# Performance work log

Hardware: AMD Instinct MI355X
Metric: run time of the kernel (lower is better)

## Reference

```python
import jax, jax.numpy as jnp
import numpy as np

N_NODES = 100000
N_EDGES = 1600000
DIM = 128
N_SEEDS = 15000


def _gcn_stack(edges, x, Ws):
    """Multi-layer GCN with sym-normalized edge-list aggregation, residual, ReLU.
    edges: [2, E] int; x: [N, d] float; Ws: list of [d, d] weights."""
    n = x.shape[0]
    loop = jnp.arange(n, dtype=edges.dtype)
    src = jnp.concatenate([edges[0], loop])  # add self-loops
    dst = jnp.concatenate([edges[1], loop])
    deg = jax.ops.segment_sum(jnp.ones(src.shape, x.dtype), dst, num_segments=n)
    dinv = jax.lax.rsqrt(deg)  # deg >= 1 thanks to self-loops
    norm = dinv[src] * dinv[dst]  # [E+N]
    for W in Ws:
        h = x @ W                                   # [N, d] dense transform
        msg = norm[:, None] * h[src]                # gather + scale, [E+N, d]
        agg = jax.ops.segment_sum(msg, dst, num_segments=n)  # scatter-add
        x = jax.nn.relu(agg + h)                    # residual + activation
    return x


def setup_inputs() -> dict:
    key = jax.random.key(0)
    ks = jax.random.split(key, 8)
    scale = 1.0 / np.sqrt(DIM)
    return {
        "sr_ent_seeds": jax.random.randint(ks[0], (N_SEEDS,), 0, N_NODES),
        "tg_ent_seeds": jax.random.randint(ks[1], (N_SEEDS,), 0, N_NODES),
        "edges_sr": jax.random.randint(ks[2], (2, N_EDGES), 0, N_NODES),
        "edges_tg": jax.random.randint(ks[3], (2, N_EDGES), 0, N_NODES),
        "embedding_sr": jax.random.normal(ks[4], (N_NODES, DIM), jnp.float32),
        "embedding_tg": jax.random.normal(ks[5], (N_NODES, DIM), jnp.float32),
        "W0": jax.random.normal(ks[6], (DIM, DIM), jnp.float32) * scale,
        "W1": jax.random.normal(ks[7], (DIM, DIM), jnp.float32) * scale,
    }


def reference(sr_ent_seeds, tg_ent_seeds, edges_sr, edges_tg,
              embedding_sr, embedding_tg, W0, W1):
    Ws = [W0, W1]
    sr_ent_hid = _gcn_stack(edges_sr, embedding_sr, Ws)
    tg_ent_hid = _gcn_stack(edges_tg, embedding_tg, Ws)
    sr_seed_hid = sr_ent_hid[sr_ent_seeds]
    tg_seed_hid = tg_ent_hid[tg_ent_seeds]
    return (sr_seed_hid, tg_seed_hid, sr_ent_hid, tg_ent_hid)
```

## Files before the change

### kernel.cpp

```cpp
#include <hip/hip_runtime.h>

#define NN 100000
#define NE 1600000
#define NT (2 * NN)
#define ET (2 * NE)
#define DIM 128
#define NS 15000
#define SB2 ((NT + 255) / 256)
#define PAD 136
#define NRANGE 16
#define RSZ (NT / NRANGE)
#define CH 16
#define BCAP 210000
#define NE4 (NE / 4)

typedef __attribute__((ext_vector_type(8))) short frag_ab;
typedef __attribute__((ext_vector_type(4))) float frag_cd;
typedef __attribute__((ext_vector_type(4))) int i4;
typedef __attribute__((ext_vector_type(2))) float f32x2;

__device__ __forceinline__ unsigned short f2bf(float f) {
    unsigned int u = __float_as_uint(f);
    u += 0x7fff + ((u >> 16) & 1);
    return (unsigned short)(u >> 16);
}
__device__ __forceinline__ float bflo(unsigned int u) { return __uint_as_float(u << 16); }
__device__ __forceinline__ float bfhi(unsigned int u) { return __uint_as_float(u & 0xffff0000u); }

__global__ __launch_bounds__(256) void bucket_k(const int* __restrict__ e_sr,
                                                const int* __restrict__ e_tg,
                                                int* __restrict__ gcur,
                                                int* __restrict__ bkt) {
    __shared__ int bcnt[4][NRANGE];
    __shared__ int bbase[4][NRANGE];
    const int tid = threadIdx.x;
    if (tid < 4 * NRANGE) ((int*)bcnt)[tid] = 0;
    __syncthreads();
    const int g = blockIdx.x * 256 + tid;
    i4 s4, d4;
    if (g < NE4) {
        s4 = *((const i4*)e_sr + g);
        d4 = *((const i4*)e_sr + NE4 + g);
    } else {
        s4 = *((const i4*)e_tg + g - NE4);
        d4 = *((const i4*)e_tg + g);
        s4 += NN;
        d4 += NN;
    }
    const int wv = tid >> 6;
    int rr[4], lr[4];
#pragma unroll
    for (int j = 0; j < 4; ++j) {
        rr[j] = d4[j] / RSZ;
        lr[j] = atomicAdd(&bcnt[wv][rr[j]], 1);
    }
    __syncthreads();
    if (tid < NRANGE) {
        const int t0 = bcnt[0][tid], t1 = bcnt[1][tid];
        const int t2 = bcnt[2][tid], t3 = bcnt[3][tid];
        const int b = atomicAdd(&gcur[tid], t0 + t1 + t2 + t3);
        bbase[0][tid] = b;
        bbase[1][tid] = b + t0;
        bbase[2][tid] = b + t0 + t1;
        bbase[3][tid] = b + t0 + t1 + t2;
    }
    __syncthreads();
#pragma unroll
    for (int j = 0; j < 4; ++j) {
        const int dtl = d4[j] - rr[j] * RSZ;
        bkt[bbase[wv][rr[j]] + lr[j]] = (dtl << 18) | s4[j];
    }
}

__global__ __launch_bounds__(1024) void hist_k(const int* __restrict__ gcur,
                                               const int* __restrict__ bkt,
                                               int* __restrict__ P) {
    __shared__ int lc[RSZ];
    const int r = blockIdx.x & (NRANGE - 1);
    const int c = blockIdx.x >> 4;
    const int lo = r * RSZ;
    for (int i = threadIdx.x; i < RSZ; i += 1024) lc[i] = 0;
    __syncthreads();
    const int n_r = gcur[r] - r * BCAP;
    const int S = (n_r + CH - 1) / CH;
    const int s0 = c * S;
    int s1 = s0 + S; if (s1 > n_r) s1 = n_r;
    for (int v = s0 + threadIdx.x; v < s1; v += 1024) {
        const unsigned int w = (unsigned int)bkt[r * BCAP + v];
        atomicAdd(&lc[w >> 18], 1);
    }
    __syncthreads();
    for (int i = threadIdx.x; i < RSZ; i += 1024) P[c * NT + lo + i] = lc[i];
}

__global__ __launch_bounds__(256) void reduceA_k(const int* __restrict__ P,
                                                 int* __restrict__ cnt,
                                                 float* __restrict__ dinv,
                                                 int* __restrict__ bsum) {
    __shared__ int sh[256];
    const int t = threadIdx.x;
    const int i = blockIdx.x * 256 + t;
    int s = 0;
    if (i < NT) {
#pragma unroll
        for (int c = 0; c < CH; ++c) s += P[c * NT + i];
        cnt[i] = s;
        dinv[i] = rsqrtf((float)(s + 1));
    }
    sh[t] = s;
    __syncthreads();
    for (int off = 128; off > 0; off >>= 1) {
        if (t < off) sh[t] += sh[t + off];
        __syncthreads();
    }
    if (t == 0) bsum[blockIdx.x] = sh[0];
}

__global__ __launch_bounds__(256) void scanCbase_k(const int* __restrict__ cnt,
                                                   const int* __restrict__ bsum,
                                                   int* __restrict__ row_ptr,
                                                   int* __restrict__ P) {
    __shared__ int s[256];
    const int t = threadIdx.x;
    const int i = blockIdx.x * 256 + t;
    int acc = 0;
    for (int b = t; b < blockIdx.x; b += 256) acc += bsum[b];
    s[t] = acc;
    __syncthreads();
    for (int off = 128; off > 0; off >>= 1) {
        if (t < off) s[t] += s[t + off];
        __syncthreads();
    }
    const int boff = s[0];
    __syncthreads();
    const int v = (i < NT) ? cnt[i] : 0;
    s[t] = v;
    __syncthreads();
    for (int off = 1; off < 256; off <<= 1) {
        int add = (t >= off) ? s[t - off] : 0;
        __syncthreads();
        s[t] += add;
        __syncthreads();
    }
    if (blockIdx.x == 0 && t == 0) row_ptr[NT] = ET;
    if (i < NT) {
        const int rp = boff + s[t] - v;
        row_ptr[i] = rp;
        int run = rp;
#pragma unroll
        for (int c = 0; c < CH; ++c) {
            const int pv = P[c * NT + i];
            P[c * NT + i] = run;
            run += pv;
        }
    }
}

__global__ __launch_bounds__(1024) void fillp_k(const int* __restrict__ gcur,
                                                const int* __restrict__ bkt,
                                                const int* __restrict__ P,
                                                int* __restrict__ csr_src) {
    __shared__ int cur[RSZ];
    const int r = blockIdx.x & (NRANGE - 1);
    const int c = blockIdx.x >> 4;
    const int lo = r * RSZ;
    for (int i = threadIdx.x; i < RSZ; i += 1024) cur[i] = P[c * NT + lo + i];
    __syncthreads();
    const int n_r = gcur[r] - r * BCAP;
    const int S = (n_r + CH - 1) / CH;
    const int s0 = c * S;
    int s1 = s0 + S; if (s1 > n_r) s1 = n_r;
    for (int v = s0 + threadIdx.x; v < s1; v += 1024) {
        const unsigned int w = (unsigned int)bkt[r * BCAP + v];
        const int pos = atomicAdd(&cur[w >> 18], 1);
        csr_src[pos] = (int)(w & 0x3FFFFu);
    }
}

__global__ __launch_bounds__(256) void convW2_k(const float* __restrict__ W0,
                                                const float* __restrict__ W1,
                                                unsigned short* __restrict__ wt0,
                                                unsigned short* __restrict__ wt1,
                                                int* __restrict__ gcur) {
    int i = blockIdx.x * 256 + threadIdx.x;
    if (blockIdx.x == 0 && threadIdx.x < NRANGE) gcur[threadIdx.x] = threadIdx.x * BCAP;
    if (i >= 2 * DIM * DIM) return;
    const float* W = (i < DIM * DIM) ? W0 : W1;
    unsigned short* wt = (i < DIM * DIM) ? wt0 : wt1;
    const int ii = i & (DIM * DIM - 1);
    const int n = ii & 127, k = ii >> 7;
    wt[n * DIM + k] = f2bf(W[k * DIM + n]);
}

__global__ __launch_bounds__(256) void gemmE_k(const float* __restrict__ emb_sr,
                                               const float* __restrict__ emb_tg,
                                               const unsigned short* __restrict__ Wt,
                                               const float* __restrict__ dinv,
                                               unsigned short* __restrict__ Gb) {
    __shared__ unsigned short xs[64 * PAD];
    __shared__ unsigned short ws[128 * PAD];
    const int tid = threadIdx.x;
    const int row0 = blockIdx.x * 64;

    for (int i = tid; i < 128 * 16; i += 256) {
        const int r = i >> 4, o = i & 15;
        *(uint4*)&ws[r * PAD + o * 8] = *(const uint4*)&Wt[r * DIM + o * 8];
    }
    for (int i = tid; i < 64 * 32; i += 256) {
        const int r = i >> 5, o = i & 31;
        const int gr = row0 + r;
        const float4 v = (gr < NN) ? ((const float4*)emb_sr)[gr * 32 + o]
                                   : ((const float4*)emb_tg)[(gr - NN) * 32 + o];
        ushort4 b;
        b.x = f2bf(v.x); b.y = f2bf(v.y); b.z = f2bf(v.z); b.w = f2bf(v.w);
        *(ushort4*)&xs[r * PAD + o * 4] = b;
    }
    __syncthreads();

    const int wave = tid >> 6;
    const int lane = tid & 63;
    const int m = lane & 15;
    const int quad = lane >> 4;
    const int rbase = wave * 16;

    frag_cd acc[8];
#pragma unroll
    for (int ct = 0; ct < 8; ct++) acc[ct] = (frag_cd){0.f, 0.f, 0.f, 0.f};

#pragma unroll
    for (int ks = 0; ks < 4; ks++) {
        const frag_ab a = *(const frag_ab*)&xs[(rbase + m) * PAD + ks * 32 + quad * 8];
#pragma unroll
        for (int ct = 0; ct < 8; ct++) {
            const frag_ab b = *(const frag_ab*)&ws[(ct * 16 + m) * PAD + ks * 32 + quad * 8];
            acc[ct] = __builtin_amdgcn_mfma_f32_16x16x32_bf16(a, b, acc[ct], 0, 0, 0);
        }
    }

#pragma unroll
    for (int r = 0; r < 4; r++) {
        const int grow = row0 + rbase + quad * 4 + r;
        const float dv = dinv[grow];
#pragma unroll
        for (int ct = 0; ct < 8; ct++)
            Gb[grow * DIM + ct * 16 + m] = f2bf(dv * acc[ct][r]);
    }
}

__global__ __launch_bounds__(256) void gemm_mfma_k(const unsigned short* __restrict__ Xb,
                                                   const unsigned short* __restrict__ Wt,
                                                   const float* __restrict__ dinv,
                                                   unsigned short* __restrict__ Gb) {
    __shared__ unsigned short xs[64 * PAD];
    __shared__ unsigned short ws[128 * PAD];
    const int tid = threadIdx.x;
    const int row0 = blockIdx.x * 64;

    for (int i = tid; i < 128 * 16; i += 256) {
        const int r = i >> 4, o = i & 15;
        *(uint4*)&ws[r * PAD + o * 8] = *(const uint4*)&Wt[r * DIM + o * 8];
    }
    for (int i = tid; i < 64 * 16; i += 256) {
        const int r = i >> 4, o = i & 15;
        *(uint4*)&xs[r * PAD + o * 8] = *(const uint4*)&Xb[(row0 + r) * DIM + o * 8];
    }
    __syncthreads();

    const int wave = tid >> 6;
    const int lane = tid & 63;
    const int m = lane & 15;
    const int quad = lane >> 4;
    const int rbase = wave * 16;

    frag_cd acc[8];
#pragma unroll
    for (int ct = 0; ct < 8; ct++) acc[ct] = (frag_cd){0.f, 0.f, 0.f, 0.f};

#pragma unroll
    for (int ks = 0; ks < 4; ks++) {
        const frag_ab a = *(const frag_ab*)&xs[(rbase + m) * PAD + ks * 32 + quad * 8];
#pragma unroll
        for (int ct = 0; ct < 8; ct++) {
            const frag_ab b = *(const frag_ab*)&ws[(ct * 16 + m) * PAD + ks * 32 + quad * 8];
            acc[ct] = __builtin_amdgcn_mfma_f32_16x16x32_bf16(a, b, acc[ct], 0, 0, 0);
        }
    }

#pragma unroll
    for (int r = 0; r < 4; r++) {
        const int grow = row0 + rbase + quad * 4 + r;
        const float dv = dinv[grow];
#pragma unroll
        for (int ct = 0; ct < 8; ct++)
            Gb[grow * DIM + ct * 16 + m] = f2bf(dv * acc[ct][r]);
    }
}

template <bool OUT_BF16>
__global__ __launch_bounds__(256) void pull_k(const int* __restrict__ row_ptr,
                                              const int* __restrict__ csr_src,
                                              const float* __restrict__ dinv,
                                              const unsigned short* __restrict__ Gb,
                                              float* __restrict__ outf,
                                              unsigned short* __restrict__ outb) {
    const int node = (blockIdx.x * 256 + threadIdx.x) >> 6;
    if (node >= NT) return;
    const int lane = threadIdx.x & 63;
    const unsigned int* __restrict__ G2 = (const unsigned int*)Gb;

    const int beg = row_ptr[node];
    const int end = row_ptr[node + 1];
    const float d = dinv[node];
    const float sq = 1.0f / d;

    const unsigned int gu = G2[node * 64 + lane];
    float sx = bflo(gu);
    float sy = bfhi(gu);
    const float hx = sx * sq;
    const float hy = sy * sq;

    for (int base = beg; base < end; base += 64) {
        int rem = end - base; if (rem > 64) rem = 64;
        const int sl = (lane < rem)
            ? __builtin_nontemporal_load(&csr_src[base + lane]) : 0;
        int j = 0;
        for (; j + 16 <= rem; j += 16) {
            int ss[16];
            unsigned int mm[16];
#pragma unroll
            for (int q = 0; q < 16; ++q) ss[q] = __shfl(sl, j + q);
#pragma unroll
            for (int q = 0; q < 16; ++q) mm[q] = G2[ss[q] * 64 + lane];
#pragma unroll
            for (int q = 0; q < 16; ++q) { sx += bflo(mm[q]); sy += bfhi(mm[q]); }
        }
        for (; j + 8 <= rem; j += 8) {
            int ss[8];
            unsigned int mm[8];
#pragma unroll
            for (int q = 0; q < 8; ++q) ss[q] = __shfl(sl, j + q);
#pragma unroll
            for (int q = 0; q < 8; ++q) mm[q] = G2[ss[q] * 64 + lane];
#pragma unroll
            for (int q = 0; q < 8; ++q) { sx += bflo(mm[q]); sy += bfhi(mm[q]); }
        }
        for (; j + 4 <= rem; j += 4) {
            int ss[4];
            unsigned int mm[4];
#pragma unroll
            for (int q = 0; q < 4; ++q) ss[q] = __shfl(sl, j + q);
#pragma unroll
            for (int q = 0; q < 4; ++q) mm[q] = G2[ss[q] * 64 + lane];
#pragma unroll
            for (int q = 0; q < 4; ++q) { sx += bflo(mm[q]); sy += bfhi(mm[q]); }
        }
        for (; j < rem; ++j) {
            const int s = __shfl(sl, j);
            const unsigned int mu = G2[s * 64 + lane];
            sx += bflo(mu);
            sy += bfhi(mu);
        }
    }
    const float ax = fmaxf(d * sx + hx, 0.f);
    const float ay = fmaxf(d * sy + hy, 0.f);
    if (OUT_BF16) {
        const unsigned int o =
            (unsigned int)f2bf(ax) | ((unsigned int)f2bf(ay) << 16);
        __builtin_nontemporal_store(o, &((unsigned int*)outb)[node * 64 + lane]);
    } else {
        f32x2 o; o.x = ax; o.y = ay;
        __builtin_nontemporal_store(o, &((f32x2*)outf)[node * 64 + lane]);
    }
}

__global__ __launch_bounds__(256) void gather2_k(const int* __restrict__ sr_seeds,
                                                 const int* __restrict__ tg_seeds,
                                                 const float* __restrict__ ent,
                                                 float* __restrict__ sr_out,
                                                 float* __restrict__ tg_out) {
    const int gid = blockIdx.x * 256 + threadIdx.x;
    const int s = gid >> 5;
    if (s >= 2 * NS) return;
    const int q = gid & 31;
    const bool tg = s >= NS;
    const int si = tg ? s - NS : s;
    const int node = tg ? tg_seeds[si] + NN : sr_seeds[si];
    float* o = tg ? tg_out : sr_out;
    ((float4*)o)[si * 32 + q] = ((const float4*)ent)[node * 32 + q];
}

extern "C" void kernel_launch(void* const* d_in, const int* in_sizes, int n_in,
                              void* d_out, int out_size, void* d_ws, size_t ws_size,
                              hipStream_t stream) {
    const int* sr_seeds = (const int*)d_in[0];
    const int* tg_seeds = (const int*)d_in[1];
    const int* edges_sr = (const int*)d_in[2];
    const int* edges_tg = (const int*)d_in[3];
    const float* emb_sr = (const float*)d_in[4];
    const float* emb_tg = (const float*)d_in[5];
    const float* W0 = (const float*)d_in[6];
    const float* W1 = (const float*)d_in[7];
    float* out = (float*)d_out;

    int* cnt = (int*)d_ws;
    float* dinv = (float*)(cnt + 200704);
    int* row_ptr = (int*)(dinv + 200704);
    int* bsum = row_ptr + 200704;
    int* csr_src = bsum + 1024;
    unsigned short* wt0 = (unsigned short*)(csr_src + ET);
    unsigned short* wt1 = wt0 + DIM * DIM;
    unsigned short* hb = wt1 + DIM * DIM;
    int* P = (int*)hb;
    int* bkt = P + CH * NT;
    int* gcur = bsum + 800;

    float* sr_seed_out = out;
    float* tg_seed_out = out + (long long)NS * DIM;
    float* ent = out + (long long)2 * NS * DIM;
    unsigned short* xb = (unsigned short*)ent;

    const int gGemm = (NT + 63) / 64;
    const int gPull = NT / 4;
    const int gBkt = ET / 1024;
    const int gHF = NRANGE * CH;

    convW2_k<<<(2 * DIM * DIM + 255) / 256, 256, 0, stream>>>(W0, W1, wt0, wt1, gcur);

    bucket_k<<<gBkt, 256, 0, stream>>>(edges_sr, edges_tg, gcur, bkt);
    hist_k<<<gHF, 1024, 0, stream>>>(gcur, bkt, P);
    reduceA_k<<<SB2, 256, 0, stream>>>(P, cnt, dinv, bsum);
    scanCbase_k<<<SB2, 256, 0, stream>>>(cnt, bsum, row_ptr, P);
    fillp_k<<<gHF, 1024, 0, stream>>>(gcur, bkt, P, csr_src);

    gemmE_k<<<gGemm, 256, 0, stream>>>(emb_sr, emb_tg, wt0, dinv, hb);
    pull_k<true><<<gPull, 256, 0, stream>>>(row_ptr, csr_src, dinv, hb, nullptr, xb);
    gemm_mfma_k<<<gGemm, 256, 0, stream>>>(xb, wt1, dinv, hb);
    pull_k<false><<<gPull, 256, 0, stream>>>(row_ptr, csr_src, dinv, hb, ent, nullptr);

    const int gSeed = (2 * NS * 32 + 255) / 256;
    gather2_k<<<gSeed, 256, 0, stream>>>(sr_seeds, tg_seeds, ent, sr_seed_out, tg_seed_out);
}
```

Baseline: 576.8 us.

## Merge CSR build kernels into one cooperative kernel with grid syncs

Replaces the six preprocessing launches (weight convert, bucket, histogram, reduce, scan, fill) with a single cooperative kernel of 256 blocks by 1024 threads that separates the phases with grid-wide syncs. Buckets now use a per-range base offset with a zeroed counter set by a memset. The goal is to remove kernel launch gaps and tail effects between the small phases. In exchange, the bucketing phase runs in grid-stride loops with extra block barriers, and the cooperative launch limits the grid to co-resident blocks.

```diff
diff --git a/kernel.cpp b/kernel.cpp
--- a/kernel.cpp
+++ b/kernel.cpp
@@ -1,4 +1,7 @@
 #include <hip/hip_runtime.h>
+#include <hip/hip_cooperative_groups.h>
+
+namespace cg = cooperative_groups;
 
 #define NN 100000
 #define NE 1600000
@@ -6,13 +9,14 @@
 #define ET (2 * NE)
 #define DIM 128
 #define NS 15000
-#define SB2 ((NT + 255) / 256)
 #define PAD 136
 #define NRANGE 16
 #define RSZ (NT / NRANGE)
 #define CH 16
 #define BCAP 210000
 #define NE4 (NE / 4)
+#define CGRID 256
+#define CTHR 1024
 
 typedef __attribute__((ext_vector_type(8))) short frag_ab;
 typedef __attribute__((ext_vector_type(4))) float frag_cd;
@@ -27,169 +31,169 @@
 __device__ __forceinline__ float bflo(unsigned int u) { return __uint_as_float(u << 16); }
 __device__ __forceinline__ float bfhi(unsigned int u) { return __uint_as_float(u & 0xffff0000u); }
 
-__global__ __launch_bounds__(256) void bucket_k(const int* __restrict__ e_sr,
-                                                const int* __restrict__ e_tg,
-                                                int* __restrict__ gcur,
-                                                int* __restrict__ bkt) {
-    __shared__ int bcnt[4][NRANGE];
-    __shared__ int bbase[4][NRANGE];
+__global__ __launch_bounds__(CTHR) void csr_coop_k(
+    const float* __restrict__ W0, const float* __restrict__ W1,
+    unsigned short* __restrict__ wt0, unsigned short* __restrict__ wt1,
+    const int* __restrict__ e_sr, const int* __restrict__ e_tg,
+    int* __restrict__ gcur, int* __restrict__ bkt, int* __restrict__ P,
+    int* __restrict__ cnt, float* __restrict__ dinv, int* __restrict__ bsum,
+    int* __restrict__ row_ptr, int* __restrict__ csr_src)
+{
+    cg::grid_group grid = cg::this_grid();
+    __shared__ int lds_i[RSZ];
+    __shared__ int bcnt[16][NRANGE];
+    __shared__ int bbase[16][NRANGE];
     const int tid = threadIdx.x;
-    if (tid < 4 * NRANGE) ((int*)bcnt)[tid] = 0;
-    __syncthreads();
-    const int g = blockIdx.x * 256 + tid;
-    i4 s4, d4;
-    if (g < NE4) {
-        s4 = *((const i4*)e_sr + g);
-        d4 = *((const i4*)e_sr + NE4 + g);
-    } else {
-        s4 = *((const i4*)e_tg + g - NE4);
-        d4 = *((const i4*)e_tg + g);
-        s4 += NN;
-        d4 += NN;
-    }
-    const int wv = tid >> 6;
-    int rr[4], lr[4];
-#pragma unroll
-    for (int j = 0; j < 4; ++j) {
-        rr[j] = d4[j] / RSZ;
-        lr[j] = atomicAdd(&bcnt[wv][rr[j]], 1);
-    }
-    __syncthreads();
-    if (tid < NRANGE) {
-        const int t0 = bcnt[0][tid], t1 = bcnt[1][tid];
-        const int t2 = bcnt[2][tid], t3 = bcnt[3][tid];
-        const int b = atomicAdd(&gcur[tid], t0 + t1 + t2 + t3);
-        bbase[0][tid] = b;
-        bbase[1][tid] = b + t0;
-        bbase[2][tid] = b + t0 + t1;
-        bbase[3][tid] = b + t0 + t1 + t2;
-    }
-    __syncthreads();
-#pragma unroll
-    for (int j = 0; j < 4; ++j) {
-        const int dtl = d4[j] - rr[j] * RSZ;
-        bkt[bbase[wv][rr[j]] + lr[j]] = (dtl << 18) | s4[j];
-    }
-}
-
-__global__ __launch_bounds__(1024) void hist_k(const int* __restrict__ gcur,
-                                               const int* __restrict__ bkt,
-                                               int* __restrict__ P) {
-    __shared__ int lc[RSZ];
-    const int r = blockIdx.x & (NRANGE - 1);
-    const int c = blockIdx.x >> 4;
-    const int lo = r * RSZ;
-    for (int i = threadIdx.x; i < RSZ; i += 1024) lc[i] = 0;
-    __syncthreads();
-    const int n_r = gcur[r] - r * BCAP;
-    const int S = (n_r + CH - 1) / CH;
-    const int s0 = c * S;
-    int s1 = s0 + S; if (s1 > n_r) s1 = n_r;
-    for (int v = s0 + threadIdx.x; v < s1; v += 1024) {
-        const unsigned int w = (unsigned int)bkt[r * BCAP + v];
-        atomicAdd(&lc[w >> 18], 1);
-    }
-    __syncthreads();
-    for (int i = threadIdx.x; i < RSZ; i += 1024) P[c * NT + lo + i] = lc[i];
-}
-
-__global__ __launch_bounds__(256) void reduceA_k(const int* __restrict__ P,
-                                                 int* __restrict__ cnt,
-                                                 float* __restrict__ dinv,
-                                                 int* __restrict__ bsum) {
-    __shared__ int sh[256];
-    const int t = threadIdx.x;
-    const int i = blockIdx.x * 256 + t;
-    int s = 0;
-    if (i < NT) {
-#pragma unroll
-        for (int c = 0; c < CH; ++c) s += P[c * NT + i];
-        cnt[i] = s;
-        dinv[i] = rsqrtf((float)(s + 1));
-    }
-    sh[t] = s;
-    __syncthreads();
-    for (int off = 128; off > 0; off >>= 1) {
-        if (t < off) sh[t] += sh[t + off];
-        __syncthreads();
-    }
-    if (t == 0) bsum[blockIdx.x] = sh[0];
-}
-
-__global__ __launch_bounds__(256) void scanCbase_k(const int* __restrict__ cnt,
-                                                   const int* __restrict__ bsum,
-                                                   int* __restrict__ row_ptr,
-                                                   int* __restrict__ P) {
-    __shared__ int s[256];
-    const int t = threadIdx.x;
-    const int i = blockIdx.x * 256 + t;
-    int acc = 0;
-    for (int b = t; b < blockIdx.x; b += 256) acc += bsum[b];
-    s[t] = acc;
-    __syncthreads();
-    for (int off = 128; off > 0; off >>= 1) {
-        if (t < off) s[t] += s[t + off];
-        __syncthreads();
-    }
-    const int boff = s[0];
-    __syncthreads();
-    const int v = (i < NT) ? cnt[i] : 0;
-    s[t] = v;
-    __syncthreads();
-    for (int off = 1; off < 256; off <<= 1) {
-        int add = (t >= off) ? s[t - off] : 0;
-        __syncthreads();
-        s[t] += add;
-        __syncthreads();
-    }
-    if (blockIdx.x == 0 && t == 0) row_ptr[NT] = ET;
-    if (i < NT) {
-        const int rp = boff + s[t] - v;
-        row_ptr[i] = rp;
-        int run = rp;
-#pragma unroll
-        for (int c = 0; c < CH; ++c) {
-            const int pv = P[c * NT + i];
-            P[c * NT + i] = run;
-            run += pv;
-        }
-    }
-}
-
-__global__ __launch_bounds__(1024) void fillp_k(const int* __restrict__ gcur,
-                                                const int* __restrict__ bkt,
-                                                const int* __restrict__ P,
-                                                int* __restrict__ csr_src) {
-    __shared__ int cur[RSZ];
-    const int r = blockIdx.x & (NRANGE - 1);
-    const int c = blockIdx.x >> 4;
-    const int lo = r * RSZ;
-    for (int i = threadIdx.x; i < RSZ; i += 1024) cur[i] = P[c * NT + lo + i];
-    __syncthreads();
-    const int n_r = gcur[r] - r * BCAP;
-    const int S = (n_r + CH - 1) / CH;
-    const int s0 = c * S;
-    int s1 = s0 + S; if (s1 > n_r) s1 = n_r;
-    for (int v = s0 + threadIdx.x; v < s1; v += 1024) {
-        const unsigned int w = (unsigned int)bkt[r * BCAP + v];
-        const int pos = atomicAdd(&cur[w >> 18], 1);
-        csr_src[pos] = (int)(w & 0x3FFFFu);
-    }
-}
-
-__global__ __launch_bounds__(256) void convW2_k(const float* __restrict__ W0,
-                                                const float* __restrict__ W1,
-                                                unsigned short* __restrict__ wt0,
-                                                unsigned short* __restrict__ wt1,
-                                                int* __restrict__ gcur) {
-    int i = blockIdx.x * 256 + threadIdx.x;
-    if (blockIdx.x == 0 && threadIdx.x < NRANGE) gcur[threadIdx.x] = threadIdx.x * BCAP;
-    if (i >= 2 * DIM * DIM) return;
-    const float* W = (i < DIM * DIM) ? W0 : W1;
-    unsigned short* wt = (i < DIM * DIM) ? wt0 : wt1;
-    const int ii = i & (DIM * DIM - 1);
-    const int n = ii & 127, k = ii >> 7;
-    wt[n * DIM + k] = f2bf(W[k * DIM + n]);
+    const int bid = blockIdx.x;
+
+    for (int i = bid * CTHR + tid; i < 2 * DIM * DIM; i += CGRID * CTHR) {
+        const float* W = (i < DIM * DIM) ? W0 : W1;
+        unsigned short* wt = (i < DIM * DIM) ? wt0 : wt1;
+        const int ii = i & (DIM * DIM - 1);
+        const int n = ii & 127, k = ii >> 7;
+        wt[n * DIM + k] = f2bf(W[k * DIM + n]);
+    }
+
+    const int NIT = (2 * NE4 + CGRID * CTHR - 1) / (CGRID * CTHR);
+    for (int it = 0; it < NIT; ++it) {
+        const int g = it * (CGRID * CTHR) + bid * CTHR + tid;
+        const bool val = g < 2 * NE4;
+        i4 s4 = {0, 0, 0, 0}, d4 = {0, 0, 0, 0};
+        if (val) {
+            if (g < NE4) {
+                s4 = *((const i4*)e_sr + g);
+                d4 = *((const i4*)e_sr + NE4 + g);
+            } else {
+                s4 = *((const i4*)e_tg + g - NE4);
+                d4 = *((const i4*)e_tg + g);
+                s4 += NN;
+                d4 += NN;
+            }
+        }
+        const int wv = tid >> 6;
+        if (tid < 16 * NRANGE) ((int*)bcnt)[tid] = 0;
+        __syncthreads();
+        int rr[4], lr[4];
+        if (val) {
+#pragma unroll
+            for (int j = 0; j < 4; ++j) {
+                rr[j] = d4[j] / RSZ;
+                lr[j] = atomicAdd(&bcnt[wv][rr[j]], 1);
+            }
+        }
+        __syncthreads();
+        if (tid < NRANGE) {
+            int tot = 0, pre[16];
+#pragma unroll
+            for (int w = 0; w < 16; ++w) { pre[w] = tot; tot += bcnt[w][tid]; }
+            const int b = atomicAdd(&gcur[tid], tot);
+#pragma unroll
+            for (int w = 0; w < 16; ++w) bbase[w][tid] = b + pre[w];
+        }
+        __syncthreads();
+        if (val) {
+#pragma unroll
+            for (int j = 0; j < 4; ++j) {
+                const int dtl = d4[j] - rr[j] * RSZ;
+                bkt[rr[j] * BCAP + bbase[wv][rr[j]] + lr[j]] = (dtl << 18) | s4[j];
+            }
+        }
+        __syncthreads();
+    }
+    grid.sync();
+
+    {
+        const int r = bid & (NRANGE - 1);
+        const int c = bid >> 4;
+        const int lo = r * RSZ;
+        for (int i = tid; i < RSZ; i += CTHR) lds_i[i] = 0;
+        __syncthreads();
+        const int n_r = gcur[r];
+        const int S = (n_r + CH - 1) / CH;
+        const int s0 = c * S;
+        int s1 = s0 + S; if (s1 > n_r) s1 = n_r;
+        for (int v = s0 + tid; v < s1; v += CTHR) {
+            const unsigned int w = (unsigned int)bkt[r * BCAP + v];
+            atomicAdd(&lds_i[w >> 18], 1);
+        }
+        __syncthreads();
+        for (int i = tid; i < RSZ; i += CTHR) P[c * NT + lo + i] = lds_i[i];
+    }
+    grid.sync();
+
+    {
+        const int i = bid * CTHR + tid;
+        int s = 0;
+        if (i < NT) {
+#pragma unroll
+            for (int c = 0; c < CH; ++c) s += P[c * NT + i];
+            cnt[i] = s;
+            dinv[i] = rsqrtf((float)(s + 1));
+        }
+        lds_i[tid] = s;
+        __syncthreads();
+        for (int off = 512; off > 0; off >>= 1) {
+            if (tid < off) lds_i[tid] += lds_i[tid + off];
+            __syncthreads();
+        }
+        if (tid == 0) bsum[bid] = lds_i[0];
+    }
+    grid.sync();
+
+    {
+        lds_i[tid] = 0;
+        __syncthreads();
+        if (tid < CGRID) lds_i[tid] = bsum[tid];
+        __syncthreads();
+        for (int off = 1; off < CGRID; off <<= 1) {
+            int add = (tid >= off && tid < CGRID) ? lds_i[tid - off] : 0;
+            __syncthreads();
+            if (tid < CGRID) lds_i[tid] += add;
+            __syncthreads();
+        }
+        const int boff = (bid == 0) ? 0 : lds_i[bid - 1];
+        __syncthreads();
+        const int i = bid * CTHR + tid;
+        const int v = (i < NT) ? cnt[i] : 0;
+        lds_i[tid] = v;
+        __syncthreads();
+        for (int off = 1; off < CTHR; off <<= 1) {
+            int add = (tid >= off) ? lds_i[tid - off] : 0;
+            __syncthreads();
+            lds_i[tid] += add;
+            __syncthreads();
+        }
+        if (bid == 0 && tid == 0) row_ptr[NT] = ET;
+        if (i < NT) {
+            const int rp = boff + lds_i[tid] - v;
+            row_ptr[i] = rp;
+            int run = rp;
+#pragma unroll
+            for (int c = 0; c < CH; ++c) {
+                const int pv = P[c * NT + i];
+                P[c * NT + i] = run;
+                run += pv;
+            }
+        }
+    }
+    grid.sync();
+
+    {
+        const int r = bid & (NRANGE - 1);
+        const int c = bid >> 4;
+        const int lo = r * RSZ;
+        for (int i = tid; i < RSZ; i += CTHR) lds_i[i] = P[c * NT + lo + i];
+        __syncthreads();
+        const int n_r = gcur[r];
+        const int S = (n_r + CH - 1) / CH;
+        const int s0 = c * S;
+        int s1 = s0 + S; if (s1 > n_r) s1 = n_r;
+        for (int v = s0 + tid; v < s1; v += CTHR) {
+            const unsigned int w = (unsigned int)bkt[r * BCAP + v];
+            const int pos = atomicAdd(&lds_i[w >> 18], 1);
+            csr_src[pos] = (int)(w & 0x3FFFFu);
+        }
+    }
 }
 
 __global__ __launch_bounds__(256) void gemmE_k(const float* __restrict__ emb_sr,
@@ -421,16 +425,17 @@
 
     const int gGemm = (NT + 63) / 64;
     const int gPull = NT / 4;
-    const int gBkt = ET / 1024;
-    const int gHF = NRANGE * CH;
-
-    convW2_k<<<(2 * DIM * DIM + 255) / 256, 256, 0, stream>>>(W0, W1, wt0, wt1, gcur);
-
-    bucket_k<<<gBkt, 256, 0, stream>>>(edges_sr, edges_tg, gcur, bkt);
-    hist_k<<<gHF, 1024, 0, stream>>>(gcur, bkt, P);
-    reduceA_k<<<SB2, 256, 0, stream>>>(P, cnt, dinv, bsum);
-    scanCbase_k<<<SB2, 256, 0, stream>>>(cnt, bsum, row_ptr, P);
-    fillp_k<<<gHF, 1024, 0, stream>>>(gcur, bkt, P, csr_src);
+
+    hipMemsetAsync(gcur, 0, NRANGE * sizeof(int), stream);
+    {
+        void* args[] = {(void*)&W0, (void*)&W1, (void*)&wt0, (void*)&wt1,
+                        (void*)&edges_sr, (void*)&edges_tg,
+                        (void*)&gcur, (void*)&bkt, (void*)&P,
+                        (void*)&cnt, (void*)&dinv, (void*)&bsum,
+                        (void*)&row_ptr, (void*)&csr_src};
+        hipLaunchCooperativeKernel((const void*)csr_coop_k, dim3(CGRID),
+                                   dim3(CTHR), args, 0, stream);
+    }
 
     gemmE_k<<<gGemm, 256, 0, stream>>>(emb_sr, emb_tg, wt0, dinv, hb);
     pull_k<true><<<gPull, 256, 0, stream>>>(row_ptr, csr_src, dinv, hb, nullptr, xb);
```

Measured after the change: 700.8 us. 1.22x slower.
